# Optimization experiments

Measured on AMD Instinct MI355X. Metric: run time of the kernel, lower is better.

## Reference

```python
import jax, jax.numpy as jnp
import numpy as np

EPS = 1e-5
POOL = 4  # two stacked AvgPool3d(2) == one AvgPool3d(4, stride=4) on the valid region


def setup_inputs() -> dict:
    key = jax.random.key(0)
    k1, k2, k3 = jax.random.split(key, 3)
    N, Cin, Cout, D = 16, 32, 16, 32
    x = jax.random.normal(k1, (N, Cin, D, D, D), dtype=jnp.float32)
    w = jax.random.normal(k2, (Cin, Cout, 3, 3, 3), dtype=jnp.float32) * 0.1
    b = jax.random.normal(k3, (Cout,), dtype=jnp.float32) * 0.1
    gamma = jnp.ones((Cout,), dtype=jnp.float32)
    beta = jnp.zeros((Cout,), dtype=jnp.float32)
    return {"x": x, "w": w, "b": b, "gamma": gamma, "beta": beta}


def _convT_bn_pool(x, w, b, gamma, beta):
    # ConvTranspose3d(stride=2, padding=1, K=3) == dilated conv with
    # lhs_dilation=2, padding=K-1-p=1, spatially-flipped kernel, IO->OI swap.
    wt = jnp.flip(w, axis=(2, 3, 4)).transpose(1, 0, 2, 3, 4)  # [Cout,Cin,3,3,3]
    y = jax.lax.conv_general_dilated(
        x, wt,
        window_strides=(1, 1, 1),
        padding=[(1, 1), (1, 1), (1, 1)],
        lhs_dilation=(2, 2, 2),
        dimension_numbers=("NCDHW", "OIDHW", "NCDHW"),
    )
    y = y + b[None, :, None, None, None]  # [N,Cout,Dout,Hout,Wout], Dout=2D-1

    # BatchNorm training stats: biased variance over (N,D,H,W) per channel
    mean = jnp.mean(y, axis=(0, 2, 3, 4), keepdims=True)
    var = jnp.mean(jnp.square(y - mean), axis=(0, 2, 3, 4), keepdims=True)
    inv = jax.lax.rsqrt(var + EPS)
    yn = (y - mean) * inv * gamma[None, :, None, None, None] + beta[None, :, None, None, None]

    # Two AvgPool3d(2) == AvgPool3d(4, stride 4) on the cropped valid region
    N_, C_, Do, Ho, Wo = yn.shape
    D2, H2, W2 = Do // POOL, Ho // POOL, Wo // POOL
    yn = yn[:, :, : D2 * POOL, : H2 * POOL, : W2 * POOL]
    yn = yn.reshape(N_, C_, D2, POOL, H2, POOL, W2, POOL)
    return jnp.mean(yn, axis=(3, 5, 7))  # [N,C,D2,H2,W2]


def reference(x, w, b, gamma, beta):
    return _convT_bn_pool(x, w, b, gamma, beta)
```

## Files before the change

kernel.cpp:

```cpp
#include <hip/hip_runtime.h>


typedef __attribute__((ext_vector_type(8))) short bf16x8;
typedef __attribute__((ext_vector_type(4))) float f32x4;

static __device__ __forceinline__ unsigned short f2bf(float f) {
    unsigned int u = __float_as_uint(f);
    u = (u + 0x7fffu + ((u >> 16) & 1u)) >> 16;
    return (unsigned short)u;
}
static __device__ __forceinline__ unsigned cvtpk(float a, float b) {
    unsigned r;
    asm("v_cvt_pk_bf16_f32 %0, %1, %2" : "=v"(r) : "v"(a), "v"(b));
    return r;
}

__global__ __launch_bounds__(256)
void kw(const float* __restrict__ w, unsigned short* __restrict__ wT)
{
    const int idx = blockIdx.x * 256 + threadIdx.x;
    if (idx < 13824) {
        const int ci = idx & 31, co = (idx >> 5) & 15, tap = idx >> 9;
        wT[idx] = f2bf(w[(ci * 16 + co) * 27 + tap]);
    }
}

__global__ __launch_bounds__(256, 4)
void convf2(const float* __restrict__ x,
            const unsigned short* __restrict__ wT,
            const float* __restrict__ bias,
            float* __restrict__ pooled,
            float* __restrict__ psum, float* __restrict__ psq)
{
    const int ht = blockIdx.x, dt = blockIdx.y, n = blockIdx.z;
    const int tid = threadIdx.x;
    const int v = tid >> 6, lane = tid & 63;
    const int t = v & 1, odp = v >> 1;
    const int c = lane & 15, qd = lane >> 4;

    __shared__ unsigned short xs[9504];
    __shared__ float sred[4][16], qred[4][16], pbuf[2][8][16];

    const int iw = tid & 31, g = (tid >> 5) & 3, half = tid >> 7;
    float f[5][8];
    #pragma unroll
    for (int p = 0; p < 5; ++p) {
        const int dihi = p * 2 + half;
        const int di = dihi / 3, hi = dihi - di * 3;
        const int id = 2*dt + di, ih = 2*ht + hi;
        const bool ok = (dihi < 9) && (id < 32) && (ih < 32);
        const float* px = x + ((((n*32 + g*8)*32 + id)*32 + ih)*32) + iw;
        #pragma unroll
        for (int j = 0; j < 8; ++j)
            f[p][j] = ok ? px[j * 32768] : 0.f;
    }
    #pragma unroll
    for (int p = 0; p < 5; ++p) {
        const int dihi = p * 2 + half;
        if (dihi < 9) {
            uint4 u;
            u.x = cvtpk(f[p][0], f[p][1]); u.y = cvtpk(f[p][2], f[p][3]);
            u.z = cvtpk(f[p][4], f[p][5]); u.w = cvtpk(f[p][6], f[p][7]);
            *(uint4*)(xs + dihi*1056 + g*264 + iw*8) = u;
        }
    }
    if (tid < 36) {
        const int dihi = tid >> 2, gg = tid & 3;
        *(uint4*)(xs + dihi*1056 + gg*264 + 256) = make_uint4(0,0,0,0);
    }

    __syncthreads();

    f32x4 acc[2][4][2];
    #pragma unroll
    for (int ol = 0; ol < 2; ++ol)
        #pragma unroll
        for (int oh = 0; oh < 4; ++oh)
            #pragma unroll
            for (int par = 0; par < 2; ++par)
                acc[ol][oh][par] = (f32x4){0.f,0.f,0.f,0.f};

    const int iwb = 16 * t + c;
    auto LDA = [&](int dihi, int sofs) -> bf16x8 {
        return *(const bf16x8*)(xs + dihi*1056 + qd*264 + (iwb + sofs)*8);
    };
    auto LDB = [&](int tap) -> bf16x8 {
        return *(const bf16x8*)(wT + tap * 512 + c * 32 + qd * 8);
    };

    constexpr int KHP[3][2][2] = {
        {{1,1},{2,3}},
        {{0,0},{1,2}},
        {{0,1},{1,3}},
    };

    auto PH = [&](int ol, int base, int di) {
        #pragma unroll
        for (int kh = 0; kh < 3; ++kh) {
            const bf16x8 B0 = LDB(base + kh*3 + 0);
            const bf16x8 B1 = LDB(base + kh*3 + 1);
            const bf16x8 B2 = LDB(base + kh*3 + 2);
            #pragma unroll
            for (int p = 0; p < 2; ++p) {
                const int hi = KHP[kh][p][0], oh = KHP[kh][p][1];
                const bf16x8 A0 = LDA(di*3 + hi, 0), A1 = LDA(di*3 + hi, 1);
                acc[ol][oh][0] = __builtin_amdgcn_mfma_f32_16x16x32_bf16(
                    A0, B1, acc[ol][oh][0], 0, 0, 0);
                acc[ol][oh][1] = __builtin_amdgcn_mfma_f32_16x16x32_bf16(
                    A1, B0, acc[ol][oh][1], 0, 0, 0);
                acc[ol][oh][1] = __builtin_amdgcn_mfma_f32_16x16x32_bf16(
                    A0, B2, acc[ol][oh][1], 0, 0, 0);
            }
        }
    };

    PH(0,  9, odp);
    PH(1, 18, odp);
    PH(1,  0, odp + 1);

    const float bv = bias[c];
    float s = 0.f, sq = 0.f;
    float P[2] = {0.f, 0.f};
    #pragma unroll
    for (int ol = 0; ol < 2; ++ol) {
        const int odg = 2*odp + ol;
        const bool odok = !(dt == 15 && odg == 3);
        #pragma unroll
        for (int oh = 0; oh < 4; ++oh) {
            const bool ohok = !(ht == 15 && oh == 3);
            #pragma unroll
            for (int par = 0; par < 2; ++par)
                #pragma unroll
                for (int r = 0; r < 4; ++r) {
                    const float val = acc[ol][oh][par][r] + bv;
                    const bool owok = !(par == 1 && t == 1 && qd == 3 && r == 3);
                    const float mk = (odok && ohok && owok) ? 1.f : 0.f;
                    s += mk * val; sq += mk * val * val;
                    P[r >> 1] += val;
                }
        }
    }
    s  += __shfl_xor(s, 16, 64);  s  += __shfl_xor(s, 32, 64);
    sq += __shfl_xor(sq, 16, 64); sq += __shfl_xor(sq, 32, 64);

    if (lane < 16) { sred[v][lane] = s; qred[v][lane] = sq; }
    if (odp == 0 && dt < 15 && ht < 15) {
        pbuf[t][2*qd + 0][c] = P[0];
        pbuf[t][2*qd + 1][c] = P[1];
    }
    __syncthreads();
    if (tid < 16) {
        const int blk = (n*16 + dt)*16 + ht;
        psum[tid*4096 + blk] = sred[0][tid]+sred[1][tid]+sred[2][tid]+sred[3][tid];
        psq [tid*4096 + blk] = qred[0][tid]+qred[1][tid]+qred[2][tid]+qred[3][tid];
    }
    if (odp == 1 && dt < 15 && ht < 15) {
        #pragma unroll
        for (int jj = 0; jj < 2; ++jj) {
            const int jl = 2*qd + jj, jg = 8*t + jl;
            if (jg < 15) {
                const float tot = pbuf[t][jl][c] + P[jj];
                pooled[(n*16 + c)*3375 + dt*225 + ht*15 + jg] = tot * (1.f/64.f);
            }
        }
    }
}

__global__ void bnfinal(const float* __restrict__ psum, const float* __restrict__ psq,
                        const float* __restrict__ gamma, const float* __restrict__ beta,
                        float* __restrict__ bn)
{
    const int co = blockIdx.x;
    const int t  = threadIdx.x;
    float S = 0, Q = 0;
    for (int blk = t; blk < 4096; blk += 256) {
        S += psum[co*4096 + blk];
        Q += psq [co*4096 + blk];
    }
    #pragma unroll
    for (int off = 32; off > 0; off >>= 1) {
        S += __shfl_down(S, off, 64);
        Q += __shfl_down(Q, off, 64);
    }
    __shared__ float rs[4], rq[4];
    if ((t & 63) == 0) { rs[t >> 6] = S; rq[t >> 6] = Q; }
    __syncthreads();
    if (t == 0) {
        S = rs[0] + rs[1] + rs[2] + rs[3];
        Q = rq[0] + rq[1] + rq[2] + rq[3];
        const float cnt = 16.f * 63.f * 63.f * 63.f;
        const float mean = S / cnt;
        const float var  = Q / cnt - mean * mean;
        const float inv  = rsqrtf(var + 1e-5f);
        const float sc   = inv * gamma[co];
        bn[co]      = sc;
        bn[16 + co] = beta[co] - mean * sc;
    }
}

__global__ void finalize(const float* __restrict__ pooled, const float* __restrict__ bn,
                         float* __restrict__ out)
{
    const int i  = blockIdx.x * 256 + threadIdx.x;
    const int co = (i / 3375) & 15;
    out[i] = pooled[i] * bn[co] + bn[16 + co];
}

extern "C" void kernel_launch(void* const* d_in, const int* in_sizes, int n_in,
                              void* d_out, int out_size, void* d_ws, size_t ws_size,
                              hipStream_t stream)
{
    const float* x     = (const float*)d_in[0];
    const float* w     = (const float*)d_in[1];
    const float* b     = (const float*)d_in[2];
    const float* gamma = (const float*)d_in[3];
    const float* beta  = (const float*)d_in[4];
    float* out = (float*)d_out;

    char* wsb = (char*)d_ws;
    unsigned short* wT = (unsigned short*)wsb;
    float* pooled = (float*)(wsb + 27648);
    float* psum   = (float*)(wsb + 27648 + 3456000);
    float* psq    = (float*)(wsb + 27648 + 3456000 + 262144);
    float* bn     = (float*)(wsb + 27648 + 3456000 + 2*262144);

    kw<<<54, 256, 0, stream>>>(w, wT);
    dim3 grid(16, 16, 16);
    convf2<<<grid, 256, 0, stream>>>(x, wT, b, pooled, psum, psq);
    bnfinal<<<16, 256, 0, stream>>>(psum, psq, gamma, beta, bn);
    finalize<<<3375, 256, 0, stream>>>(pooled, bn, out);
}
```

Measured before the change: 142.3 us.

## Vectorize input staging with float4 loads and lane shuffles; prefetch weight fragments

Input staging now has each thread issue float4 loads along the w axis for one input channel, instead of scalar loads strided across channels. Cross-lane shuffles and byte permutes then reassemble the channel-interleaved bf16 layout in shared memory. The goal is fewer, wider, coalesced global loads. Separately, the MFMA loop now loads the next step's weight B-fragments from global memory one step ahead to hide their latency, at the cost of extra registers and shuffle instructions.

```diff
diff --git a/kernel.cpp b/kernel.cpp
--- a/kernel.cpp
+++ b/kernel.cpp
@@ -41,28 +41,35 @@
     __shared__ unsigned short xs[9504];
     __shared__ float sred[4][16], qred[4][16], pbuf[2][8][16];
 
-    const int iw = tid & 31, g = (tid >> 5) & 3, half = tid >> 7;
-    float f[5][8];
-    #pragma unroll
-    for (int p = 0; p < 5; ++p) {
-        const int dihi = p * 2 + half;
-        const int di = dihi / 3, hi = dihi - di * 3;
+    const float bv = bias[c];
+
+    const int ciS = tid >> 3, q = tid & 7;
+    const int oL = ciS & 7;
+    const float* xbase = x + (n*32 + ciS)*32768 + 4*q;
+    float4 F[9];
+    #pragma unroll
+    for (int p = 0; p < 9; ++p) {
+        const int di = p / 3, hi = p - 3*(p/3);
         const int id = 2*dt + di, ih = 2*ht + hi;
-        const bool ok = (dihi < 9) && (id < 32) && (ih < 32);
-        const float* px = x + ((((n*32 + g*8)*32 + id)*32 + ih)*32) + iw;
-        #pragma unroll
-        for (int j = 0; j < 8; ++j)
-            f[p][j] = ok ? px[j * 32768] : 0.f;
-    }
-    #pragma unroll
-    for (int p = 0; p < 5; ++p) {
-        const int dihi = p * 2 + half;
-        if (dihi < 9) {
-            uint4 u;
-            u.x = cvtpk(f[p][0], f[p][1]); u.y = cvtpk(f[p][2], f[p][3]);
-            u.z = cvtpk(f[p][4], f[p][5]); u.w = cvtpk(f[p][6], f[p][7]);
-            *(uint4*)(xs + dihi*1056 + g*264 + iw*8) = u;
-        }
+        const bool ok = (id < 32) && (ih < 32);
+        F[p] = ok ? *(const float4*)(xbase + id*1024 + ih*32)
+                  : make_float4(0.f, 0.f, 0.f, 0.f);
+    }
+    const unsigned selP = (lane & 8) ? 0x07060302u : 0x01000504u;
+    const int iwT = 4*q + (oL & 3), hT = oL >> 2;
+    #pragma unroll
+    for (int p = 0; p < 9; ++p) {
+        unsigned u0 = cvtpk(F[p].x, F[p].y);
+        unsigned u1 = cvtpk(F[p].z, F[p].w);
+        const unsigned a0 = (unsigned)__shfl_xor((int)u0, 8, 64);
+        const unsigned a1 = (unsigned)__shfl_xor((int)u1, 8, 64);
+        u0 = __builtin_amdgcn_perm(u0, a0, selP);
+        u1 = __builtin_amdgcn_perm(u1, a1, selP);
+        const unsigned t0 = (unsigned)__shfl_xor((int)u0, 16, 64);
+        const unsigned t1 = (unsigned)__shfl_xor((int)u1, 16, 64);
+        const unsigned n0 = (lane & 16) ? t1 : u0;
+        const unsigned n1 = (lane & 16) ? u1 : t0;
+        *(uint2*)(xs + p*1056 + v*264 + iwT*8 + 4*hT) = make_uint2(n0, n1);
     }
     if (tid < 36) {
         const int dihi = tid >> 2, gg = tid & 3;
@@ -93,32 +100,36 @@
         {{0,0},{1,2}},
         {{0,1},{1,3}},
     };
-
-    auto PH = [&](int ol, int base, int di) {
-        #pragma unroll
-        for (int kh = 0; kh < 3; ++kh) {
-            const bf16x8 B0 = LDB(base + kh*3 + 0);
-            const bf16x8 B1 = LDB(base + kh*3 + 1);
-            const bf16x8 B2 = LDB(base + kh*3 + 2);
-            #pragma unroll
-            for (int p = 0; p < 2; ++p) {
-                const int hi = KHP[kh][p][0], oh = KHP[kh][p][1];
-                const bf16x8 A0 = LDA(di*3 + hi, 0), A1 = LDA(di*3 + hi, 1);
-                acc[ol][oh][0] = __builtin_amdgcn_mfma_f32_16x16x32_bf16(
-                    A0, B1, acc[ol][oh][0], 0, 0, 0);
-                acc[ol][oh][1] = __builtin_amdgcn_mfma_f32_16x16x32_bf16(
-                    A1, B0, acc[ol][oh][1], 0, 0, 0);
-                acc[ol][oh][1] = __builtin_amdgcn_mfma_f32_16x16x32_bf16(
-                    A0, B2, acc[ol][oh][1], 0, 0, 0);
-            }
-        }
-    };
-
-    PH(0,  9, odp);
-    PH(1, 18, odp);
-    PH(1,  0, odp + 1);
-
-    const float bv = bias[c];
+    const int PB[3]  = {9, 18, 0};
+    const int POL[3] = {0, 1, 1};
+    const int PDI[3] = {odp, odp, odp + 1};
+
+    bf16x8 B0 = LDB(9 + 0), B1 = LDB(9 + 1), B2 = LDB(9 + 2);
+    #pragma unroll
+    for (int s = 0; s < 9; ++s) {
+        const int ph = s / 3, kh = s - 3*(s/3);
+        bf16x8 N0, N1, N2;
+        if (s < 8) {
+            const int sn = s + 1;
+            const int phn = sn / 3, khn = sn - 3*(sn/3);
+            const int bn_ = PB[phn] + khn * 3;
+            N0 = LDB(bn_ + 0); N1 = LDB(bn_ + 1); N2 = LDB(bn_ + 2);
+        }
+        const int ol = POL[ph], di = PDI[ph];
+        #pragma unroll
+        for (int pp = 0; pp < 2; ++pp) {
+            const int hi = KHP[kh][pp][0], oh = KHP[kh][pp][1];
+            const bf16x8 A0 = LDA(di*3 + hi, 0), A1 = LDA(di*3 + hi, 1);
+            acc[ol][oh][0] = __builtin_amdgcn_mfma_f32_16x16x32_bf16(
+                A0, B1, acc[ol][oh][0], 0, 0, 0);
+            acc[ol][oh][1] = __builtin_amdgcn_mfma_f32_16x16x32_bf16(
+                A1, B0, acc[ol][oh][1], 0, 0, 0);
+            acc[ol][oh][1] = __builtin_amdgcn_mfma_f32_16x16x32_bf16(
+                A0, B2, acc[ol][oh][1], 0, 0, 0);
+        }
+        if (s < 8) { B0 = N0; B1 = N1; B2 = N2; }
+    }
+
     float s = 0.f, sq = 0.f;
     float P[2] = {0.f, 0.f};
     #pragma unroll
```

Result: faster. 137.2 us (-3.6%).
